# Optimization experiments

Hardware: AMD Instinct MI355X
Metric: run time of the kernel (lower is better)

Reference implementation:

```python
import jax, jax.numpy as jnp
import numpy as np

B, S, D = 2, 2048, 1024
H = 16
DH = D // H  # 64

def setup_inputs() -> dict:
    key = jax.random.key(0)
    k1, k2, k3, k4 = jax.random.split(key, 4)
    scale = 0.02
    x = jax.random.normal(k1, (B, S, D), dtype=jnp.float32)
    W_query = jax.random.normal(k2, (D, D), dtype=jnp.float32) * scale
    W_key = jax.random.normal(k3, (D, D), dtype=jnp.float32) * scale
    W_value = jax.random.normal(k4, (D, D), dtype=jnp.float32) * scale
    return {"x": x, "W_query": W_query, "W_key": W_key, "W_value": W_value}

def reference(x, W_query, W_key, W_value):
    b, n, d_in = x.shape
    # project and split heads: [b, h, n, dh]
    q = (x @ W_query).reshape(b, n, H, DH).transpose(0, 2, 1, 3)
    k = (x @ W_key).reshape(b, n, H, DH).transpose(0, 2, 1, 3)
    v = (x @ W_value).reshape(b, n, H, DH).transpose(0, 2, 1, 3)
    # raw scores, then causal mask (strict upper triangle -> -inf)
    scores = jnp.einsum('bhqd,bhkd->bhqk', q, k)
    causal = jnp.tril(jnp.ones((n, n), dtype=bool))  # True = keep
    scores = jnp.where(causal, scores, -jnp.inf)
    weights = jax.nn.softmax(scores / jnp.sqrt(jnp.float32(DH)), axis=-1)
    ctx = jnp.einsum('bhqk,bhkd->bhqd', weights, v)
    return ctx.transpose(0, 2, 1, 3).reshape(b, n, H * DH)
```

## Files before the change

### kernel.cpp

```cpp
#include <hip/hip_runtime.h>
#include <hip/hip_bf16.h>

#define S_LEN   2048
#define D_MODEL 1024
#define N_HEADS 16
#define D_HEAD  64
#define HEAD_ELEMS (2048ull * 64ull)
#define MAT_ELEMS  (4096ull * 1024ull)
#define W_ELEMS    (1024ull * 1024ull)

typedef __attribute__((ext_vector_type(8))) short short8_t;
typedef __attribute__((ext_vector_type(4))) short short4_t;
typedef __attribute__((ext_vector_type(4))) float f32x4;

__device__ __forceinline__ short f2bf(float f) {
    __hip_bfloat16 h = __float2bfloat16(f);
    union { __hip_bfloat16 h; short s; } cv;
    cv.h = h;
    return cv.s;
}

#define GLD_LDS16(gptr, lptr) \
    __builtin_amdgcn_global_load_lds( \
        (const __attribute__((address_space(1))) unsigned int*)(gptr), \
        (__attribute__((address_space(3))) unsigned int*)(lptr), 16, 0, 0)

__global__ __launch_bounds__(256) void convert_x_kernel(
    const float* __restrict__ x, short* __restrict__ xb)
{
    const int i = (blockIdx.x * 256 + threadIdx.x) * 8;
    const float4 v0 = *(const float4*)(x + i);
    const float4 v1 = *(const float4*)(x + i + 4);
    short8_t u;
    u[0] = f2bf(v0.x); u[1] = f2bf(v0.y); u[2] = f2bf(v0.z); u[3] = f2bf(v0.w);
    u[4] = f2bf(v1.x); u[5] = f2bf(v1.y); u[6] = f2bf(v1.z); u[7] = f2bf(v1.w);
    *(short8_t*)(xb + i) = u;
}

__global__ __launch_bounds__(256) void transpose_w_kernel(
    const float* __restrict__ Wq, const float* __restrict__ Wk,
    const float* __restrict__ Wv, short* __restrict__ wt)
{
    const int k0 = blockIdx.x * 64;
    const int n0 = blockIdx.y * 64;
    const int which = blockIdx.z;
    const float* W = (which == 0) ? Wq : (which == 1) ? Wk : Wv;
    short* out = wt + (size_t)which * W_ELEMS;

    __shared__ float Ts[64][68];
    const int t = threadIdx.x;
    {
        const int c4 = (t & 15) * 4;
#pragma unroll
        for (int i = 0; i < 4; ++i) {
            const int r = (t >> 4) + i * 16;
            const float4 v = *(const float4*)(W + (size_t)(k0 + r) * D_MODEL + n0 + c4);
            Ts[c4 + 0][r] = v.x; Ts[c4 + 1][r] = v.y;
            Ts[c4 + 2][r] = v.z; Ts[c4 + 3][r] = v.w;
        }
    }
    __syncthreads();
    const int nl = t >> 2;
#pragma unroll
    for (int s = 0; s < 2; ++s) {
        const int koff = (t & 3) * 8 + s * 32;
        short8_t u;
#pragma unroll
        for (int j = 0; j < 8; ++j) u[j] = f2bf(Ts[nl][koff + j]);
        *(short8_t*)(out + (size_t)(n0 + nl) * D_MODEL + k0 + koff) = u;
    }
}

__global__ __launch_bounds__(256, 3) void qkv_mfma_gemm_kernel(
    const short* __restrict__ xb,
    const short* __restrict__ wt,
    short* __restrict__ qkv)
{
    const int mBlock = blockIdx.x * 128;
    const int nBlock = blockIdx.y * 128;
    const int which  = blockIdx.z;
    const short* Bt = wt + (size_t)which * W_ELEMS;
    short* outBase  = qkv + (size_t)which * MAT_ELEMS;

    __shared__ short As[128 * 32];
    __shared__ short Bs[128 * 32];

    const int t    = threadIdx.x;
    const int w    = t >> 6;
    const int lane = t & 63;
    const int n16  = lane & 15;
    const int quad = lane >> 4;
    const int mq   = (w & 1) * 64;
    const int nq   = (w >> 1) * 64;

    f32x4 acc[4][4];
#pragma unroll
    for (int i = 0; i < 4; ++i)
#pragma unroll
        for (int j = 0; j < 4; ++j) acc[i][j] = (f32x4){0.f, 0.f, 0.f, 0.f};

    const int off0 = w * 2048 + lane * 16;
    const int off1 = off0 + 1024;
    const int r0s = off0 >> 6, k0s = (off0 & 63) >> 1;
    const int r1s = off1 >> 6, k1s = (off1 & 63) >> 1;
    const short* gA0 = xb + (size_t)(mBlock + r0s) * D_MODEL + k0s;
    const short* gA1 = xb + (size_t)(mBlock + r1s) * D_MODEL + k1s;
    const short* gB0 = Bt + (size_t)(nBlock + r0s) * D_MODEL + k0s;
    const short* gB1 = Bt + (size_t)(nBlock + r1s) * D_MODEL + k1s;
    short* lA0 = As + w * 1024;
    short* lA1 = As + w * 1024 + 512;
    short* lB0 = Bs + w * 1024;
    short* lB1 = Bs + w * 1024 + 512;

    for (int k0 = 0; k0 < D_MODEL; k0 += 32) {
        __syncthreads();
        GLD_LDS16(gA0 + k0, lA0);
        GLD_LDS16(gA1 + k0, lA1);
        GLD_LDS16(gB0 + k0, lB0);
        GLD_LDS16(gB1 + k0, lB1);
        __syncthreads();

        short8_t af[4], bf[4];
#pragma unroll
        for (int mt = 0; mt < 4; ++mt)
            af[mt] = *(const short8_t*)&As[(mq + mt * 16 + n16) * 32 + quad * 8];
#pragma unroll
        for (int nt = 0; nt < 4; ++nt)
            bf[nt] = *(const short8_t*)&Bs[(nq + nt * 16 + n16) * 32 + quad * 8];
#pragma unroll
        for (int mt = 0; mt < 4; ++mt)
#pragma unroll
            for (int nt = 0; nt < 4; ++nt)
                acc[mt][nt] = __builtin_amdgcn_mfma_f32_16x16x32_bf16(
                    af[mt], bf[nt], acc[mt][nt], 0, 0, 0);
    }

    const float oscale = (which == 0) ? 0.125f * 1.44269504089f : 1.0f;
    if (which < 2) {
#pragma unroll
        for (int mt = 0; mt < 4; ++mt) {
#pragma unroll
            for (int nt = 0; nt < 4; ++nt) {
                const int n = nBlock + nq + nt * 16 + n16;
                const int h = n >> 6, dh = n & 63;
#pragma unroll
                for (int reg = 0; reg < 4; ++reg) {
                    const int m = mBlock + mq + mt * 16 + quad * 4 + reg;
                    const int bb = m >> 11, ss = m & 2047;
                    outBase[((size_t)(bb * N_HEADS + h) * S_LEN + ss) * D_HEAD + dh] =
                        f2bf(acc[mt][nt][reg] * oscale);
                }
            }
        }
    } else {
#pragma unroll
        for (int mt = 0; mt < 4; ++mt) {
            const int m0 = mBlock + mq + mt * 16 + quad * 4;
            const int bb = m0 >> 11, ss0 = m0 & 2047;
#pragma unroll
            for (int nt = 0; nt < 4; ++nt) {
                const int n = nBlock + nq + nt * 16 + n16;
                const int h = n >> 6, dh = n & 63;
                short4_t u;
                u[0] = f2bf(acc[mt][nt][0]); u[1] = f2bf(acc[mt][nt][1]);
                u[2] = f2bf(acc[mt][nt][2]); u[3] = f2bf(acc[mt][nt][3]);
                *(short4_t*)(outBase +
                    ((size_t)((bb * N_HEADS + h) * D_HEAD + dh)) * S_LEN + ss0) = u;
            }
        }
    }
}

__global__ __launch_bounds__(256, 2) void attn_mfma_kernel(
    const short* __restrict__ qkv,
    float* __restrict__ out)
{
    const int bh   = blockIdx.x;
    const int pr   = blockIdx.y;
    const int t    = threadIdx.x;
    const int w    = t >> 6;
    const int lane = t & 63;
    const int n    = lane & 15;
    const int quad = lane >> 4;

    const short* Q  = qkv + (size_t)bh * HEAD_ELEMS;
    const short* K  = qkv + MAT_ELEMS + (size_t)bh * HEAD_ELEMS;
    const short* Vt = qkv + 2 * MAT_ELEMS + (size_t)bh * HEAD_ELEMS;

    __shared__ __align__(16) short Ks[2][64 * 64];
    __shared__ __align__(16) short Vs[2][64 * 64];
    __shared__ __align__(16) short Ps[4][16][72];

    const int srow0 = w * 16 + (lane >> 3);
    const int srow1 = srow0 + 8;
    const int sd0 = ((lane & 7) ^ (srow0 & 7)) * 8;
    const int sd1 = ((lane & 7) ^ (srow1 & 7)) * 8;
    const short* gK0 = K + srow0 * 64 + sd0;
    const short* gK1 = K + srow1 * 64 + sd1;
    const short* gV0 = Vt + (size_t)srow0 * S_LEN + sd0;
    const short* gV1 = Vt + (size_t)srow1 * S_LEN + sd1;
    const int lo0 = (w * 16) * 64;
    const int lo1 = (w * 16 + 8) * 64;

    const int pcK = ((quad ^ (n & 7))) * 8;

    const int bb = bh >> 4;
    const int hh = bh & 15;

    for (int pass = 0; pass < 2; ++pass) {
        const int qb = pass ? (31 - pr) : pr;
        const int r0 = qb * 64 + w * 16;
        const int qrow = r0 + n;

        const short8_t bq0 = *(const short8_t*)(Q + (size_t)qrow * D_HEAD + quad * 8);
        const short8_t bq1 = *(const short8_t*)(Q + (size_t)qrow * D_HEAD + quad * 8 + 32);

        float m = -__builtin_inff();
        float l = 0.f;
        f32x4 o[4];
#pragma unroll
        for (int f = 0; f < 4; ++f) o[f] = (f32x4){0.f, 0.f, 0.f, 0.f};

        GLD_LDS16(gK0, &Ks[0][lo0]);
        GLD_LDS16(gK1, &Ks[0][lo1]);
        GLD_LDS16(gV0, &Vs[0][lo0]);
        GLD_LDS16(gV1, &Vs[0][lo1]);
        __syncthreads();

        for (int tile = 0; tile <= qb; ++tile) {
            const int cur = tile & 1;
            if (tile < qb) {
                const int j1 = (tile + 1) * 64;
                GLD_LDS16(gK0 + j1 * 64, &Ks[cur ^ 1][lo0]);
                GLD_LDS16(gK1 + j1 * 64, &Ks[cur ^ 1][lo1]);
                GLD_LDS16(gV0 + j1,      &Vs[cur ^ 1][lo0]);
                GLD_LDS16(gV1 + j1,      &Vs[cur ^ 1][lo1]);
            }
            const int j0 = tile * 64;
            const short* Kc = Ks[cur];
            const short* Vc = Vs[cur];

            f32x4 st[4];
            __builtin_amdgcn_s_setprio(1);
#pragma unroll
            for (int kg = 0; kg < 4; ++kg) {
                const int rbase = (kg * 16 + n) * 64;
                const short8_t a0 = *(const short8_t*)&Kc[rbase + pcK];
                const short8_t a1 = *(const short8_t*)&Kc[rbase + (pcK ^ 32)];
                f32x4 acc = (f32x4){0.f, 0.f, 0.f, 0.f};
                acc = __builtin_amdgcn_mfma_f32_16x16x32_bf16(a0, bq0, acc, 0, 0, 0);
                acc = __builtin_amdgcn_mfma_f32_16x16x32_bf16(a1, bq1, acc, 0, 0, 0);
                st[kg] = acc;
            }
            __builtin_amdgcn_s_setprio(0);

            float p[16];
            float mx = -__builtin_inff();
            if (tile == qb) {
#pragma unroll
                for (int kg = 0; kg < 4; ++kg)
#pragma unroll
                    for (int r = 0; r < 4; ++r) {
                        const int key = j0 + kg * 16 + quad * 4 + r;
                        float s = st[kg][r];
                        s = (key <= qrow) ? s : -__builtin_inff();
                        p[kg * 4 + r] = s;
                        mx = fmaxf(mx, s);
                    }
            } else {
#pragma unroll
                for (int i = 0; i < 16; ++i) {
                    const float s = st[i >> 2][i & 3];
                    p[i] = s;
                    mx = fmaxf(mx, s);
                }
            }
            mx = fmaxf(mx, __shfl_xor(mx, 16));
            mx = fmaxf(mx, __shfl_xor(mx, 32));

            float ls = 0.f;
            if (__all(mx <= m + 8.0f)) {
#pragma unroll
                for (int i = 0; i < 16; ++i) {
                    p[i] = __builtin_amdgcn_exp2f(p[i] - m);
                    ls += p[i];
                }
                ls += __shfl_xor(ls, 16);
                ls += __shfl_xor(ls, 32);
                l += ls;
            } else {
                const float mnew  = fmaxf(m, mx);
                const float alpha = __builtin_amdgcn_exp2f(m - mnew);
#pragma unroll
                for (int i = 0; i < 16; ++i) {
                    p[i] = __builtin_amdgcn_exp2f(p[i] - mnew);
                    ls += p[i];
                }
                ls += __shfl_xor(ls, 16);
                ls += __shfl_xor(ls, 32);
                l = l * alpha + ls;
                m = mnew;
#pragma unroll
                for (int f = 0; f < 4; ++f) {
                    o[f][0] *= alpha; o[f][1] *= alpha;
                    o[f][2] *= alpha; o[f][3] *= alpha;
                }
            }

#pragma unroll
            for (int kg = 0; kg < 4; ++kg) {
                const unsigned int b0 = __builtin_bit_cast(unsigned int, p[kg * 4 + 0]);
                const unsigned int b1 = __builtin_bit_cast(unsigned int, p[kg * 4 + 1]);
                const unsigned int b2 = __builtin_bit_cast(unsigned int, p[kg * 4 + 2]);
                const unsigned int b3 = __builtin_bit_cast(unsigned int, p[kg * 4 + 3]);
                uint2 pk;
                pk.x = (b0 >> 16) | (b1 & 0xffff0000u);
                pk.y = (b2 >> 16) | (b3 & 0xffff0000u);
                *(uint2*)&Ps[w][n][kg * 16 + quad * 4] = pk;
            }
            const short8_t pb0 = *(const short8_t*)&Ps[w][n][quad * 8];
            const short8_t pb1 = *(const short8_t*)&Ps[w][n][quad * 8 + 32];

            __builtin_amdgcn_s_setprio(1);
#pragma unroll
            for (int f = 0; f < 4; ++f) {
                const int rbase = (f * 16 + n) * 64;
                const short8_t va0 = *(const short8_t*)&Vc[rbase + pcK];
                const short8_t va1 = *(const short8_t*)&Vc[rbase + (pcK ^ 32)];
                o[f] = __builtin_amdgcn_mfma_f32_16x16x32_bf16(va0, pb0, o[f], 0, 0, 0);
                o[f] = __builtin_amdgcn_mfma_f32_16x16x32_bf16(va1, pb1, o[f], 0, 0, 0);
            }
            __builtin_amdgcn_s_setprio(0);

            __syncthreads();
        }

        float* Os = (float*)((w < 2) ? (void*)Ks : (void*)Vs) + (w & 1) * 1024;
        const float inv_l = 1.0f / l;
#pragma unroll
        for (int f = 0; f < 4; ++f) {
            const int c  = f * 4 + quad;
            const int pc = c ^ n;
            f32x4 q4;
            q4[0] = o[f][0] * inv_l; q4[1] = o[f][1] * inv_l;
            q4[2] = o[f][2] * inv_l; q4[3] = o[f][3] * inv_l;
            *(f32x4*)&Os[n * 64 + pc * 4] = q4;
        }
#pragma unroll
        for (int rr = 0; rr < 4; ++rr) {
            const int row = rr * 4 + quad;
            const int pc  = n ^ row;
            const f32x4 val = *(const f32x4*)&Os[row * 64 + pc * 4];
            *(f32x4*)(out + ((size_t)(bb * S_LEN + r0 + row)) * D_MODEL
                          + hh * D_HEAD + n * 4) = val;
        }
        __syncthreads();
    }
}

extern "C" void kernel_launch(void* const* d_in, const int* in_sizes, int n_in,
                              void* d_out, int out_size, void* d_ws, size_t ws_size,
                              hipStream_t stream) {
    const float* x  = (const float*)d_in[0];
    const float* Wq = (const float*)d_in[1];
    const float* Wk = (const float*)d_in[2];
    const float* Wv = (const float*)d_in[3];
    float* out = (float*)d_out;

    short* xb  = (short*)d_ws;
    short* wt  = xb + MAT_ELEMS;
    short* qkv = wt + 3 * W_ELEMS;

    convert_x_kernel<<<dim3(MAT_ELEMS / (256 * 8)), 256, 0, stream>>>(x, xb);
    transpose_w_kernel<<<dim3(16, 16, 3), 256, 0, stream>>>(Wq, Wk, Wv, wt);

    qkv_mfma_gemm_kernel<<<dim3(32, 8, 3), 256, 0, stream>>>(xb, wt, qkv);

    attn_mfma_kernel<<<dim3(2 * N_HEADS, 16), 256, 0, stream>>>(qkv, out);
}
```

Measured before the change: 153.7 us.

## Load K/V directly from global into registers and drop paired-pass scheduling

The attention kernel stops staging K and V tiles through double-buffered shared memory. Each wave now loads its own MFMA operands straight from global memory into registers, which removes the per-tile barriers. The grid grows to one block per 64-row query tile, launched longest-first in place of pairing a short and a long tile per block, and launch bounds are raised to 3 blocks per CU. In exchange, each of the four waves re-reads the same K/V data through cache rather than sharing it in LDS, and global load latency is no longer hidden by prefetch.

```diff
diff --git a/kernel.cpp b/kernel.cpp
--- a/kernel.cpp
+++ b/kernel.cpp
@@ -171,12 +171,12 @@
     }
 }
 
-__global__ __launch_bounds__(256, 2) void attn_mfma_kernel(
+__global__ __launch_bounds__(256, 3) void attn_mfma_kernel(
     const short* __restrict__ qkv,
     float* __restrict__ out)
 {
     const int bh   = blockIdx.x;
-    const int pr   = blockIdx.y;
+    const int qb   = 31 - blockIdx.y;
     const int t    = threadIdx.x;
     const int w    = t >> 6;
     const int lane = t & 63;
@@ -187,174 +187,149 @@
     const short* K  = qkv + MAT_ELEMS + (size_t)bh * HEAD_ELEMS;
     const short* Vt = qkv + 2 * MAT_ELEMS + (size_t)bh * HEAD_ELEMS;
 
-    __shared__ __align__(16) short Ks[2][64 * 64];
-    __shared__ __align__(16) short Vs[2][64 * 64];
     __shared__ __align__(16) short Ps[4][16][72];
-
-    const int srow0 = w * 16 + (lane >> 3);
-    const int srow1 = srow0 + 8;
-    const int sd0 = ((lane & 7) ^ (srow0 & 7)) * 8;
-    const int sd1 = ((lane & 7) ^ (srow1 & 7)) * 8;
-    const short* gK0 = K + srow0 * 64 + sd0;
-    const short* gK1 = K + srow1 * 64 + sd1;
-    const short* gV0 = Vt + (size_t)srow0 * S_LEN + sd0;
-    const short* gV1 = Vt + (size_t)srow1 * S_LEN + sd1;
-    const int lo0 = (w * 16) * 64;
-    const int lo1 = (w * 16 + 8) * 64;
-
-    const int pcK = ((quad ^ (n & 7))) * 8;
+    __shared__ __align__(16) float Os[4][16][64];
 
     const int bb = bh >> 4;
     const int hh = bh & 15;
 
-    for (int pass = 0; pass < 2; ++pass) {
-        const int qb = pass ? (31 - pr) : pr;
-        const int r0 = qb * 64 + w * 16;
-        const int qrow = r0 + n;
-
-        const short8_t bq0 = *(const short8_t*)(Q + (size_t)qrow * D_HEAD + quad * 8);
-        const short8_t bq1 = *(const short8_t*)(Q + (size_t)qrow * D_HEAD + quad * 8 + 32);
-
-        float m = -__builtin_inff();
-        float l = 0.f;
-        f32x4 o[4];
-#pragma unroll
-        for (int f = 0; f < 4; ++f) o[f] = (f32x4){0.f, 0.f, 0.f, 0.f};
-
-        GLD_LDS16(gK0, &Ks[0][lo0]);
-        GLD_LDS16(gK1, &Ks[0][lo1]);
-        GLD_LDS16(gV0, &Vs[0][lo0]);
-        GLD_LDS16(gV1, &Vs[0][lo1]);
-        __syncthreads();
-
-        for (int tile = 0; tile <= qb; ++tile) {
-            const int cur = tile & 1;
-            if (tile < qb) {
-                const int j1 = (tile + 1) * 64;
-                GLD_LDS16(gK0 + j1 * 64, &Ks[cur ^ 1][lo0]);
-                GLD_LDS16(gK1 + j1 * 64, &Ks[cur ^ 1][lo1]);
-                GLD_LDS16(gV0 + j1,      &Vs[cur ^ 1][lo0]);
-                GLD_LDS16(gV1 + j1,      &Vs[cur ^ 1][lo1]);
-            }
-            const int j0 = tile * 64;
-            const short* Kc = Ks[cur];
-            const short* Vc = Vs[cur];
-
-            f32x4 st[4];
-            __builtin_amdgcn_s_setprio(1);
-#pragma unroll
-            for (int kg = 0; kg < 4; ++kg) {
-                const int rbase = (kg * 16 + n) * 64;
-                const short8_t a0 = *(const short8_t*)&Kc[rbase + pcK];
-                const short8_t a1 = *(const short8_t*)&Kc[rbase + (pcK ^ 32)];
-                f32x4 acc = (f32x4){0.f, 0.f, 0.f, 0.f};
-                acc = __builtin_amdgcn_mfma_f32_16x16x32_bf16(a0, bq0, acc, 0, 0, 0);
-                acc = __builtin_amdgcn_mfma_f32_16x16x32_bf16(a1, bq1, acc, 0, 0, 0);
-                st[kg] = acc;
-            }
-            __builtin_amdgcn_s_setprio(0);
-
-            float p[16];
-            float mx = -__builtin_inff();
-            if (tile == qb) {
-#pragma unroll
-                for (int kg = 0; kg < 4; ++kg)
-#pragma unroll
-                    for (int r = 0; r < 4; ++r) {
-                        const int key = j0 + kg * 16 + quad * 4 + r;
-                        float s = st[kg][r];
-                        s = (key <= qrow) ? s : -__builtin_inff();
-                        p[kg * 4 + r] = s;
-                        mx = fmaxf(mx, s);
-                    }
-            } else {
-#pragma unroll
-                for (int i = 0; i < 16; ++i) {
-                    const float s = st[i >> 2][i & 3];
-                    p[i] = s;
+    const int r0   = qb * 64 + w * 16;
+    const int qrow = r0 + n;
+
+    const short8_t bq0 = *(const short8_t*)(Q + (size_t)qrow * D_HEAD + quad * 8);
+    const short8_t bq1 = *(const short8_t*)(Q + (size_t)qrow * D_HEAD + quad * 8 + 32);
+
+    const short* kbase = K + (size_t)n * D_HEAD + quad * 8;
+    const short* vbase = Vt + (size_t)n * S_LEN + quad * 8;
+
+    float m = -__builtin_inff();
+    float l = 0.f;
+    f32x4 o[4];
+#pragma unroll
+    for (int f = 0; f < 4; ++f) o[f] = (f32x4){0.f, 0.f, 0.f, 0.f};
+
+    for (int tile = 0; tile <= qb; ++tile) {
+        const int j0 = tile * 64;
+
+        short8_t ka0[4], ka1[4], va0[4], va1[4];
+#pragma unroll
+        for (int kg = 0; kg < 4; ++kg) {
+            const short* p = kbase + (size_t)(j0 + kg * 16) * D_HEAD;
+            ka0[kg] = *(const short8_t*)(p);
+            ka1[kg] = *(const short8_t*)(p + 32);
+        }
+#pragma unroll
+        for (int f = 0; f < 4; ++f) {
+            const short* p = vbase + (size_t)(f * 16) * S_LEN + j0;
+            va0[f] = *(const short8_t*)(p);
+            va1[f] = *(const short8_t*)(p + 32);
+        }
+
+        f32x4 st[4];
+        __builtin_amdgcn_s_setprio(1);
+#pragma unroll
+        for (int kg = 0; kg < 4; ++kg) {
+            f32x4 acc = (f32x4){0.f, 0.f, 0.f, 0.f};
+            acc = __builtin_amdgcn_mfma_f32_16x16x32_bf16(ka0[kg], bq0, acc, 0, 0, 0);
+            acc = __builtin_amdgcn_mfma_f32_16x16x32_bf16(ka1[kg], bq1, acc, 0, 0, 0);
+            st[kg] = acc;
+        }
+        __builtin_amdgcn_s_setprio(0);
+
+        float p[16];
+        float mx = -__builtin_inff();
+        if (tile == qb) {
+#pragma unroll
+            for (int kg = 0; kg < 4; ++kg)
+#pragma unroll
+                for (int r = 0; r < 4; ++r) {
+                    const int key = j0 + kg * 16 + quad * 4 + r;
+                    float s = st[kg][r];
+                    s = (key <= qrow) ? s : -__builtin_inff();
+                    p[kg * 4 + r] = s;
                     mx = fmaxf(mx, s);
                 }
-            }
-            mx = fmaxf(mx, __shfl_xor(mx, 16));
-            mx = fmaxf(mx, __shfl_xor(mx, 32));
-
-            float ls = 0.f;
-            if (__all(mx <= m + 8.0f)) {
-#pragma unroll
-                for (int i = 0; i < 16; ++i) {
-                    p[i] = __builtin_amdgcn_exp2f(p[i] - m);
-                    ls += p[i];
-                }
-                ls += __shfl_xor(ls, 16);
-                ls += __shfl_xor(ls, 32);
-                l += ls;
-            } else {
-                const float mnew  = fmaxf(m, mx);
-                const float alpha = __builtin_amdgcn_exp2f(m - mnew);
-#pragma unroll
-                for (int i = 0; i < 16; ++i) {
-                    p[i] = __builtin_amdgcn_exp2f(p[i] - mnew);
-                    ls += p[i];
-                }
-                ls += __shfl_xor(ls, 16);
-                ls += __shfl_xor(ls, 32);
-                l = l * alpha + ls;
-                m = mnew;
-#pragma unroll
-                for (int f = 0; f < 4; ++f) {
-                    o[f][0] *= alpha; o[f][1] *= alpha;
-                    o[f][2] *= alpha; o[f][3] *= alpha;
-                }
-            }
-
-#pragma unroll
-            for (int kg = 0; kg < 4; ++kg) {
-                const unsigned int b0 = __builtin_bit_cast(unsigned int, p[kg * 4 + 0]);
-                const unsigned int b1 = __builtin_bit_cast(unsigned int, p[kg * 4 + 1]);
-                const unsigned int b2 = __builtin_bit_cast(unsigned int, p[kg * 4 + 2]);
-                const unsigned int b3 = __builtin_bit_cast(unsigned int, p[kg * 4 + 3]);
-                uint2 pk;
-                pk.x = (b0 >> 16) | (b1 & 0xffff0000u);
-                pk.y = (b2 >> 16) | (b3 & 0xffff0000u);
-                *(uint2*)&Ps[w][n][kg * 16 + quad * 4] = pk;
-            }
-            const short8_t pb0 = *(const short8_t*)&Ps[w][n][quad * 8];
-            const short8_t pb1 = *(const short8_t*)&Ps[w][n][quad * 8 + 32];
-
-            __builtin_amdgcn_s_setprio(1);
+        } else {
+#pragma unroll
+            for (int i = 0; i < 16; ++i) {
+                const float s = st[i >> 2][i & 3];
+                p[i] = s;
+                mx = fmaxf(mx, s);
+            }
+        }
+        mx = fmaxf(mx, __shfl_xor(mx, 16));
+        mx = fmaxf(mx, __shfl_xor(mx, 32));
+
+        float ls = 0.f;
+        if (__all(mx <= m + 8.0f)) {
+#pragma unroll
+            for (int i = 0; i < 16; ++i) {
+                p[i] = __builtin_amdgcn_exp2f(p[i] - m);
+                ls += p[i];
+            }
+            ls += __shfl_xor(ls, 16);
+            ls += __shfl_xor(ls, 32);
+            l += ls;
+        } else {
+            const float mnew  = fmaxf(m, mx);
+            const float alpha = __builtin_amdgcn_exp2f(m - mnew);
+#pragma unroll
+            for (int i = 0; i < 16; ++i) {
+                p[i] = __builtin_amdgcn_exp2f(p[i] - mnew);
+                ls += p[i];
+            }
+            ls += __shfl_xor(ls, 16);
+            ls += __shfl_xor(ls, 32);
+            l = l * alpha + ls;
+            m = mnew;
 #pragma unroll
             for (int f = 0; f < 4; ++f) {
-                const int rbase = (f * 16 + n) * 64;
-                const short8_t va0 = *(const short8_t*)&Vc[rbase + pcK];
-                const short8_t va1 = *(const short8_t*)&Vc[rbase + (pcK ^ 32)];
-                o[f] = __builtin_amdgcn_mfma_f32_16x16x32_bf16(va0, pb0, o[f], 0, 0, 0);
-                o[f] = __builtin_amdgcn_mfma_f32_16x16x32_bf16(va1, pb1, o[f], 0, 0, 0);
-            }
-            __builtin_amdgcn_s_setprio(0);
-
-            __syncthreads();
-        }
-
-        float* Os = (float*)((w < 2) ? (void*)Ks : (void*)Vs) + (w & 1) * 1024;
-        const float inv_l = 1.0f / l;
+                o[f][0] *= alpha; o[f][1] *= alpha;
+                o[f][2] *= alpha; o[f][3] *= alpha;
+            }
+        }
+
+#pragma unroll
+        for (int kg = 0; kg < 4; ++kg) {
+            const unsigned int b0 = __builtin_bit_cast(unsigned int, p[kg * 4 + 0]);
+            const unsigned int b1 = __builtin_bit_cast(unsigned int, p[kg * 4 + 1]);
+            const unsigned int b2 = __builtin_bit_cast(unsigned int, p[kg * 4 + 2]);
+            const unsigned int b3 = __builtin_bit_cast(unsigned int, p[kg * 4 + 3]);
+            uint2 pk;
+            pk.x = (b0 >> 16) | (b1 & 0xffff0000u);
+            pk.y = (b2 >> 16) | (b3 & 0xffff0000u);
+            *(uint2*)&Ps[w][n][kg * 16 + quad * 4] = pk;
+        }
+        const short8_t pb0 = *(const short8_t*)&Ps[w][n][quad * 8];
+        const short8_t pb1 = *(const short8_t*)&Ps[w][n][quad * 8 + 32];
+
+        __builtin_amdgcn_s_setprio(1);
 #pragma unroll
         for (int f = 0; f < 4; ++f) {
-            const int c  = f * 4 + quad;
-            const int pc = c ^ n;
-            f32x4 q4;
-            q4[0] = o[f][0] * inv_l; q4[1] = o[f][1] * inv_l;
-            q4[2] = o[f][2] * inv_l; q4[3] = o[f][3] * inv_l;
-            *(f32x4*)&Os[n * 64 + pc * 4] = q4;
-        }
-#pragma unroll
-        for (int rr = 0; rr < 4; ++rr) {
-            const int row = rr * 4 + quad;
-            const int pc  = n ^ row;
-            const f32x4 val = *(const f32x4*)&Os[row * 64 + pc * 4];
-            *(f32x4*)(out + ((size_t)(bb * S_LEN + r0 + row)) * D_MODEL
-                          + hh * D_HEAD + n * 4) = val;
-        }
-        __syncthreads();
+            o[f] = __builtin_amdgcn_mfma_f32_16x16x32_bf16(va0[f], pb0, o[f], 0, 0, 0);
+            o[f] = __builtin_amdgcn_mfma_f32_16x16x32_bf16(va1[f], pb1, o[f], 0, 0, 0);
+        }
+        __builtin_amdgcn_s_setprio(0);
+    }
+
+    float* Osw = &Os[w][0][0];
+    const float inv_l = 1.0f / l;
+#pragma unroll
+    for (int f = 0; f < 4; ++f) {
+        const int c  = f * 4 + quad;
+        const int pc = c ^ n;
+        f32x4 q4;
+        q4[0] = o[f][0] * inv_l; q4[1] = o[f][1] * inv_l;
+        q4[2] = o[f][2] * inv_l; q4[3] = o[f][3] * inv_l;
+        *(f32x4*)&Osw[n * 64 + pc * 4] = q4;
+    }
+#pragma unroll
+    for (int rr = 0; rr < 4; ++rr) {
+        const int row = rr * 4 + quad;
+        const int pc  = n ^ row;
+        const f32x4 val = *(const f32x4*)&Osw[row * 64 + pc * 4];
+        *(f32x4*)(out + ((size_t)(bb * S_LEN + r0 + row)) * D_MODEL
+                      + hh * D_HEAD + n * 4) = val;
     }
 }
 
@@ -376,5 +351,5 @@
 
     qkv_mfma_gemm_kernel<<<dim3(32, 8, 3), 256, 0, stream>>>(xb, wt, qkv);
 
-    attn_mfma_kernel<<<dim3(2 * N_HEADS, 16), 256, 0, stream>>>(qkv, out);
-}
+    attn_mfma_kernel<<<dim3(32, 32), 256, 0, stream>>>(qkv, out);
+}
```

Result: slower. 254.6 us (+65.6%).
